# Optimization experiments

Hardware: AMD Instinct MI355X
Metric: run time of the kernel (lower is better)

The kernel has to match this reference:

```python
import jax, jax.numpy as jnp
import numpy as np
from jax import lax

C, NH, HC, HID, P = 192, 8, 64, 512, 16
B, H, W = 2, 128, 128
EPS = 1e-5


def setup_inputs() -> dict:
    key = jax.random.key(0)
    ks = jax.random.split(key, 12)
    f = lambda i, shape: jax.random.normal(ks[i], shape, jnp.float32) * 0.05
    return dict(
        x=jax.random.normal(ks[0], (B, C, H, W), jnp.float32),
        ln1_g=jnp.ones((C,), jnp.float32), ln1_b=jnp.zeros((C,), jnp.float32),
        wq=f(1, (HID, C)), wk=f(2, (HID, C)), wv=f(3, (HID, C)),
        wo=f(4, (C, HID)), bo=jnp.zeros((C,), jnp.float32),
        dw_w=f(5, (C, 1, 3, 3)), dw_b=jnp.zeros((C,), jnp.float32),
        mlp_w=f(6, (C, 2 * C)), mlp_b=jnp.zeros((C,), jnp.float32),
        ln2_g=jnp.ones((C,), jnp.float32), ln2_b=jnp.zeros((C,), jnp.float32),
        c1_w=f(7, (C, C)), c1_b=jnp.zeros((C,), jnp.float32),
        res_w=f(8, (C, 1, 3, 3)), res_b=jnp.zeros((C,), jnp.float32),
        c2_w=f(9, (C, C)), c2_b=jnp.zeros((C,), jnp.float32),
    )


def ln_ch(x, g, b):
    # LayerNorm over the channel dim of an NCHW tensor (biased variance, like torch)
    m = x.mean(1, keepdims=True)
    v = ((x - m) ** 2).mean(1, keepdims=True)
    return (x - m) / jnp.sqrt(v + EPS) * g[None, :, None, None] + b[None, :, None, None]


def inorm(x):
    # InstanceNorm2d, affine=False
    m = x.mean((2, 3), keepdims=True)
    v = ((x - m) ** 2).mean((2, 3), keepdims=True)
    return (x - m) / jnp.sqrt(v + EPS)


def conv1x1(x, w, b=None):
    y = jnp.einsum('oc,bchw->bohw', w, x)
    return y if b is None else y + b[None, :, None, None]


def dwconv(x, w, b):
    y = lax.conv_general_dilated(x, w, (1, 1), 'SAME',
                                 feature_group_count=x.shape[1],
                                 dimension_numbers=('NCHW', 'OIHW', 'NCHW'))
    return y + b[None, :, None, None]


def res_block(x, w, b):
    return jax.nn.gelu(inorm(dwconv(x, w, b)), approximate=False) + x


def dpsa(x, ln_g, ln_b, wq, wk, wv, wo, bo):
    Bs, _, Hs, Ws = x.shape
    xn = ln_ch(x, ln_g, ln_b)

    def proj(w):  # -> (B*NH, H, W, HC)
        t = jnp.einsum('oc,bchw->bohw', w, xn)
        return t.reshape(Bs * NH, HC, Hs, Ws).transpose(0, 2, 3, 1)

    l2n = lambda t: t / jnp.maximum(jnp.linalg.norm(t, axis=-1, keepdims=True), 1e-12)
    q = l2n(proj(wq))
    k = l2n(proj(wk))
    v = proj(wv)

    qs = q.sum((1, 2))                                   # (BH, HC)
    h_scores = jnp.einsum('bc,bhc->bh', qs, k.sum(2))    # (BH, H)
    w_scores = jnp.einsum('bc,bwc->bw', qs, k.sum(1))    # (BH, W)
    _, h_idx = lax.top_k(h_scores, P)
    _, w_idx = lax.top_k(w_scores, P)

    k = jnp.take_along_axis(k, h_idx[:, :, None, None], axis=1)   # (BH, P, W, HC)
    v = jnp.take_along_axis(v, h_idx[:, :, None, None], axis=1)
    k = jnp.take_along_axis(k, w_idx[:, None, :, None], axis=2)   # (BH, P, P, HC)
    v = jnp.take_along_axis(v, w_idx[:, None, :, None], axis=2)

    qf = q.reshape(Bs * NH, Hs * Ws, HC)
    kf = k.reshape(Bs * NH, P * P, HC)
    vf = v.reshape(Bs * NH, P * P, HC)
    attn = jax.nn.softmax(jnp.einsum('bqc,bkc->bqk', qf, kf), axis=-1)
    out = jnp.einsum('bqk,bkc->bqc', attn, vf)
    out = out.reshape(Bs, NH, Hs, Ws, HC).transpose(0, 1, 4, 2, 3).reshape(Bs, NH * HC, Hs, Ws)
    return conv1x1(out, wo, bo)


def reference(x, ln1_g, ln1_b, wq, wk, wv, wo, bo, dw_w, dw_b, mlp_w, mlp_b,
              ln2_g, ln2_b, c1_w, c1_b, res_w, res_b, c2_w, c2_b):
    global_branch = dpsa(x, ln1_g, ln1_b, wq, wk, wv, wo, bo)
    local_branch = dwconv(x, dw_w, dw_b)
    f = jnp.concatenate((local_branch, global_branch), axis=1)
    f = conv1x1(f, mlp_w, mlp_b) + x
    y = ln_ch(f, ln2_g, ln2_b)
    y = jax.nn.gelu(inorm(conv1x1(y, c1_w, c1_b)), approximate=False)
    y = res_block(y, res_w, res_b)
    y = inorm(conv1x1(y, c2_w, c2_b))
    return y
```

## Files before the change

### kernel.cpp

```cpp
#include <hip/hip_runtime.h>
#include <math.h>

constexpr int kC   = 192;
constexpr int kNH  = 8;
constexpr int kHC  = 64;
constexpr int kHID = 512;
constexpr int kP   = 16;
constexpr int kB   = 2;
constexpr int kH   = 128;
constexpr int kW   = 128;
constexpr int kHW  = kH * kW;
constexpr int kN   = kB * kHW;
constexpr float kEPS = 1e-5f;

typedef __attribute__((ext_vector_type(8))) short bf16x8;
typedef __attribute__((ext_vector_type(4))) float f32x4;

__device__ inline unsigned short f2bf(float f) {
    unsigned int u = __builtin_bit_cast(unsigned int, f);
    unsigned int r = (u + 0x7FFFu + ((u >> 16) & 1u)) >> 16;
    return (unsigned short)r;
}
__device__ inline float bf2f(unsigned short u) {
    return __builtin_bit_cast(float, (unsigned int)u << 16);
}
__device__ inline unsigned int cvtpk(float lo, float hi) {
    unsigned int r;
    asm("v_cvt_pk_bf16_f32 %0, %1, %2" : "=v"(r) : "v"(lo), "v"(hi));
    return r;
}
__device__ inline unsigned long long pk4(float a, float b, float c, float d) {
    return (unsigned long long)cvtpk(a, b) | ((unsigned long long)cvtpk(c, d) << 32);
}
__device__ inline f32x4 ubf4(unsigned long long u) {
    f32x4 r;
    r[0] = bf2f((unsigned short)u);
    r[1] = bf2f((unsigned short)(u >> 16));
    r[2] = bf2f((unsigned short)(u >> 32));
    r[3] = bf2f((unsigned short)(u >> 48));
    return r;
}
__device__ inline float gelu_f(float x) {
    return 0.5f * x * (1.0f + erff(x * 0.70710678118654752f));
}

__global__ void prep_kernel(float* __restrict__ zbase,
                            const float* wq, const float* wk, const float* wm,
                            const float* c1, const float* c2,
                            const float* wo, const float* mlp_b, const float* bo,
                            unsigned short* wqb, unsigned short* wkb,
                            unsigned short* mlpb1, unsigned short* c1b, unsigned short* c2b,
                            unsigned short* w2pb, float* bp2)
{
    int i = blockIdx.x * 256 + threadIdx.x;
    if (i < 2304) { zbase[i] = 0.f; return; }
    i -= 2304;
    if (i < 98304) { wqb[i] = f2bf(wq[i]); return; }
    i -= 98304;
    if (i < 98304) { wkb[i] = f2bf(wk[i]); return; }
    i -= 98304;
    if (i < 36864) { int o = i / 192, k = i - o * 192; mlpb1[i] = f2bf(wm[o * 384 + k]); return; }
    i -= 36864;
    if (i < 36864) { c1b[i] = f2bf(c1[i]); return; }
    i -= 36864;
    if (i < 36864) { c2b[i] = f2bf(c2[i]); return; }
    i -= 36864;
    if (i < 98304) {
        int o = i >> 9, j = i & 511;
        const float* a = wm + o * 384 + 192;
        float s = 0.f;
        for (int c = 0; c < 192; ++c) s += a[c] * wo[c * 512 + j];
        w2pb[o * 512 + j] = f2bf(s);
        if (j == 0) {
            float t = mlp_b[o];
            for (int c = 0; c < 192; ++c) t += a[c] * bo[c];
            bp2[o] = t;
        }
    }
}

__global__ __launch_bounds__(256) void txln_kernel(const float* __restrict__ x,
                                                   unsigned short* __restrict__ xpb,
                                                   unsigned short* __restrict__ xnb,
                                                   const float* __restrict__ g,
                                                   const float* __restrict__ bb)
{
    __shared__ float tile[192][65];
    __shared__ float red[2][4][64];
    __shared__ float pms[64], prs[64];
    int hw0 = blockIdx.x * 64;
    int b   = blockIdx.y;
    int tid = threadIdx.x;
    for (int i = tid; i < 192 * 64; i += 256) {
        int c = i >> 6, p = i & 63;
        tile[c][p] = x[(size_t)(b * kC + c) * kHW + hw0 + p];
    }
    __syncthreads();
    {
        int p = tid & 63, qt = tid >> 6;
        float s = 0.f, ss = 0.f;
        for (int c = qt * 48; c < qt * 48 + 48; ++c) {
            float v = tile[c][p]; s += v; ss += v * v;
        }
        red[0][qt][p] = s; red[1][qt][p] = ss;
    }
    __syncthreads();
    if (tid < 64) {
        float s  = red[0][0][tid] + red[0][1][tid] + red[0][2][tid] + red[0][3][tid];
        float ss = red[1][0][tid] + red[1][1][tid] + red[1][2][tid] + red[1][3][tid];
        float m = s * (1.0f / kC);
        float var = ss * (1.0f / kC) - m * m;
        pms[tid] = m;
        prs[tid] = rsqrtf(var + kEPS);
    }
    __syncthreads();
    for (int i = tid; i < 64 * 192; i += 256) {
        int p = i / 192, c = i - p * 192;
        float raw = tile[c][p];
        size_t oi = (size_t)(b * kHW + hw0 + p) * kC + c;
        xpb[oi] = f2bf(raw);
        xnb[oi] = f2bf((raw - pms[p]) * prs[p] * g[c] + bb[c]);
    }
}

#define MGEMM_CORE(KVAL, APTR, BPTR)                                              \
    {                                                                             \
        const unsigned short* Ap = APTR;                                          \
        const unsigned short* Bp = BPTR;                                          \
        _Pragma("unroll 2")                                                       \
        for (int k = 0; k < KVAL; k += 32) {                                      \
            bf16x8 a0 = *(const bf16x8*)(Ap + k);                                 \
            bf16x8 a1 = *(const bf16x8*)(Ap + (size_t)16 * KVAL + k);             \
            bf16x8 b0 = *(const bf16x8*)(Bp + k);                                 \
            bf16x8 b1 = *(const bf16x8*)(Bp + (size_t)16 * KVAL + k);             \
            bf16x8 b2 = *(const bf16x8*)(Bp + (size_t)32 * KVAL + k);             \
            bf16x8 b3 = *(const bf16x8*)(Bp + (size_t)48 * KVAL + k);             \
            acc[0][0] = __builtin_amdgcn_mfma_f32_16x16x32_bf16(a0, b0, acc[0][0], 0, 0, 0); \
            acc[0][1] = __builtin_amdgcn_mfma_f32_16x16x32_bf16(a0, b1, acc[0][1], 0, 0, 0); \
            acc[0][2] = __builtin_amdgcn_mfma_f32_16x16x32_bf16(a0, b2, acc[0][2], 0, 0, 0); \
            acc[0][3] = __builtin_amdgcn_mfma_f32_16x16x32_bf16(a0, b3, acc[0][3], 0, 0, 0); \
            acc[1][0] = __builtin_amdgcn_mfma_f32_16x16x32_bf16(a1, b0, acc[1][0], 0, 0, 0); \
            acc[1][1] = __builtin_amdgcn_mfma_f32_16x16x32_bf16(a1, b1, acc[1][1], 0, 0, 0); \
            acc[1][2] = __builtin_amdgcn_mfma_f32_16x16x32_bf16(a1, b2, acc[1][2], 0, 0, 0); \
            acc[1][3] = __builtin_amdgcn_mfma_f32_16x16x32_bf16(a1, b3, acc[1][3], 0, 0, 0); \
        }                                                                         \
    }

__global__ __launch_bounds__(256) void qk_proj_kernel(
    const unsigned short* __restrict__ wqb, const unsigned short* __restrict__ wkb,
    const unsigned short* __restrict__ xnb,
    unsigned short* __restrict__ qpb, unsigned short* __restrict__ kpb,
    float* __restrict__ qpart, float* __restrict__ ksum_h)
{
    __shared__ float rbuf[2][2][4][4][4];
    int bid = blockIdx.x;
    int xcd = bid & 7;
    int idx = bid >> 3;
    int nblk = xcd * 32 + (idx & 31);
    int hpz  = idx >> 5;
    int hp = hpz & 3, isK = hpz >> 2;

    int nB = nblk * 128;
    const unsigned short* A = isK ? wkb : wqb;
    unsigned short* out = isK ? kpb : qpb;
    float* red_out = isK ? ksum_h : qpart;

    int w = threadIdx.x >> 6, lane = threadIdx.x & 63;
    int l15 = lane & 15, g = lane >> 4;
    int wm = w & 1, wn = w >> 1;
    int oB = hp * 128;

    const unsigned short* Ap = A + (size_t)(oB + wm * 64 + l15) * 192 + 8 * g;
    const unsigned short* Bp = xnb + (size_t)(nB + wn * 64 + l15) * 192 + 8 * g;

    f32x4 acc[4][4];
#pragma unroll
    for (int mt = 0; mt < 4; ++mt)
#pragma unroll
        for (int nt = 0; nt < 4; ++nt) acc[mt][nt] = (f32x4){0.f,0.f,0.f,0.f};

#pragma unroll 2
    for (int k = 0; k < 192; k += 32) {
        bf16x8 a[4], bb[4];
#pragma unroll
        for (int mt = 0; mt < 4; ++mt) a[mt] = *(const bf16x8*)(Ap + (size_t)mt * 16 * 192 + k);
#pragma unroll
        for (int nt = 0; nt < 4; ++nt) bb[nt] = *(const bf16x8*)(Bp + (size_t)nt * 16 * 192 + k);
#pragma unroll
        for (int mt = 0; mt < 4; ++mt)
#pragma unroll
            for (int nt = 0; nt < 4; ++nt)
                acc[mt][nt] = __builtin_amdgcn_mfma_f32_16x16x32_bf16(a[mt], bb[nt], acc[mt][nt], 0, 0, 0);
    }

    float sc[4];
#pragma unroll
    for (int nt = 0; nt < 4; ++nt) {
        float s = 0.f;
#pragma unroll
        for (int mt = 0; mt < 4; ++mt) {
            f32x4 a = acc[mt][nt];
            s += (a[0]*a[0] + a[1]*a[1]) + (a[2]*a[2] + a[3]*a[3]);
        }
        s += __shfl_xor(s, 16);
        s += __shfl_xor(s, 32);
        sc[nt] = 1.0f / fmaxf(sqrtf(s), 1e-12f);
    }

#pragma unroll
    for (int nt = 0; nt < 4; ++nt) {
        int n = nB + wn * 64 + nt * 16 + l15;
#pragma unroll
        for (int mt = 0; mt < 4; ++mt) {
            int o = oB + wm * 64 + mt * 16 + 4 * g;
            f32x4 v = acc[mt][nt];
            *(unsigned long long*)(out + (size_t)n * kHID + o) =
                pk4(v[0]*sc[nt], v[1]*sc[nt], v[2]*sc[nt], v[3]*sc[nt]);
        }
    }

    float sred[4][4] = {};
#pragma unroll
    for (int nt = 0; nt < 4; ++nt)
#pragma unroll
        for (int mt = 0; mt < 4; ++mt) {
            f32x4 a = acc[mt][nt];
            sred[mt][0] += a[0] * sc[nt];
            sred[mt][1] += a[1] * sc[nt];
            sred[mt][2] += a[2] * sc[nt];
            sred[mt][3] += a[3] * sc[nt];
        }
#pragma unroll
    for (int off = 1; off < 16; off <<= 1)
#pragma unroll
        for (int mt = 0; mt < 4; ++mt)
#pragma unroll
            for (int r = 0; r < 4; ++r)
                sred[mt][r] += __shfl_xor(sred[mt][r], off);
    if (l15 == 0)
#pragma unroll
        for (int mt = 0; mt < 4; ++mt)
#pragma unroll
            for (int r = 0; r < 4; ++r)
                rbuf[wm][wn][g][mt][r] = sred[mt][r];
    __syncthreads();
    if (threadIdx.x < 128) {
        int wm2 = threadIdx.x >> 6;
        int o = threadIdx.x & 63;
        int mt2 = o >> 4, g2 = (o >> 2) & 3, r2 = o & 3;
        float v = rbuf[wm2][0][g2][mt2][r2] + rbuf[wm2][1][g2][mt2][r2];
        int row = (nB & (kHW - 1)) >> 7;
        int b = nB >> 14;
        int bh = b * 8 + hp * 2 + wm2;
        red_out[((size_t)(bh * 128 + row)) * 64 + o] = v;
    }
}

__global__ void dwconv_pm_kernel(const unsigned short* __restrict__ in,
                                 unsigned short* __restrict__ out,
                                 const float* __restrict__ wt, const float* __restrict__ bias)
{
    int idx = blockIdx.x * 256 + threadIdx.x;
    int n = idx / 48;
    int c0 = (idx - n * 48) * 4;
    int hw = n & (kHW - 1);
    int h = hw >> 7, ww = hw & 127;
    f32x4 s = *(const f32x4*)(bias + c0);
#pragma unroll
    for (int dy = -1; dy <= 1; ++dy) {
        int hh = h + dy;
        if (hh < 0 || hh >= kH) continue;
#pragma unroll
        for (int dx = -1; dx <= 1; ++dx) {
            int wx = ww + dx;
            if (wx < 0 || wx >= kW) continue;
            f32x4 v = ubf4(*(const unsigned long long*)(in + (size_t)(n + dy * kW + dx) * kC + c0));
            int t = (dy + 1) * 3 + (dx + 1);
            s[0] += v[0] * wt[(c0 + 0) * 9 + t];
            s[1] += v[1] * wt[(c0 + 1) * 9 + t];
            s[2] += v[2] * wt[(c0 + 2) * 9 + t];
            s[3] += v[3] * wt[(c0 + 3) * 9 + t];
        }
    }
    *(unsigned long long*)(out + (size_t)n * kC + c0) = pk4(s[0], s[1], s[2], s[3]);
}

__global__ void sum_h_kernel(const unsigned short* __restrict__ buf, float* __restrict__ out)
{
    __shared__ float red[4][64];
    int w = blockIdx.x, bh = blockIdx.y;
    int hc = threadIdx.x & 63, seg = threadIdx.x >> 6;
    int b = bh >> 3, nh = bh & 7;
    const unsigned short* p = buf + (size_t)(b * kHW + seg * 32 * kW + w) * kHID + nh * kHC + hc;
    float s = 0.f;
    for (int h = 0; h < 32; ++h) s += bf2f(p[(size_t)h * kW * kHID]);
    red[seg][hc] = s;
    __syncthreads();
    if (threadIdx.x < 64)
        out[((size_t)bh * kW + w) * kHC + threadIdx.x] =
            red[0][threadIdx.x] + red[1][threadIdx.x] + red[2][threadIdx.x] + red[3][threadIdx.x];
}

__global__ __launch_bounds__(256) void mgemm_is_kernel(
    const unsigned short* __restrict__ A, const unsigned short* __restrict__ B,
    unsigned short* __restrict__ out, const float* __restrict__ bias,
    float* __restrict__ accp)
{
    __shared__ float sa[2][64], qa[2][64];
    int bid = blockIdx.x;
    int xcd = bid & 7;
    int idx = bid >> 3;
    int nB = (xcd * 32 + (idx & 31)) * 128;
    int oB = (idx >> 5) * 64;
    int w = threadIdx.x >> 6, lane = threadIdx.x & 63;
    int l15 = lane & 15, g = lane >> 4;
    int wm = w & 1, wn = w >> 1;

    f32x4 acc[2][4];
#pragma unroll
    for (int mt = 0; mt < 2; ++mt)
#pragma unroll
        for (int nt = 0; nt < 4; ++nt) acc[mt][nt] = (f32x4){0.f,0.f,0.f,0.f};

    MGEMM_CORE(192, A + (size_t)(oB + wm * 32 + l15) * 192 + 8 * g,
                    B + (size_t)(nB + wn * 64 + l15) * 192 + 8 * g);

    f32x4 vv[2][4];
#pragma unroll
    for (int mt = 0; mt < 2; ++mt)
#pragma unroll
        for (int nt = 0; nt < 4; ++nt) {
            int o = oB + wm * 32 + mt * 16 + 4 * g;
            int n = nB + wn * 64 + nt * 16 + l15;
            f32x4 v = acc[mt][nt] + *(const f32x4*)(bias + o);
            vv[mt][nt] = v;
            *(unsigned long long*)(out + (size_t)n * kC + o) = pk4(v[0], v[1], v[2], v[3]);
        }
    float s2[2][4] = {}, q2[2][4] = {};
#pragma unroll
    for (int mt = 0; mt < 2; ++mt)
#pragma unroll
        for (int nt = 0; nt < 4; ++nt)
#pragma unroll
            for (int r = 0; r < 4; ++r) {
                float v = vv[mt][nt][r];
                s2[mt][r] += v; q2[mt][r] += v * v;
            }
#pragma unroll
    for (int off = 1; off < 16; off <<= 1)
#pragma unroll
        for (int mt = 0; mt < 2; ++mt)
#pragma unroll
            for (int r = 0; r < 4; ++r) {
                s2[mt][r] += __shfl_xor(s2[mt][r], off);
                q2[mt][r] += __shfl_xor(q2[mt][r], off);
            }
    if (l15 == 0)
#pragma unroll
        for (int mt = 0; mt < 2; ++mt)
#pragma unroll
            for (int r = 0; r < 4; ++r) {
                int ol = wm * 32 + mt * 16 + 4 * g + r;
                sa[wn][ol] = s2[mt][r];
                qa[wn][ol] = q2[mt][r];
            }
    __syncthreads();
    if (threadIdx.x < 128) {
        int ol = threadIdx.x & 63, st = threadIdx.x >> 6;
        float v = st ? (qa[0][ol] + qa[1][ol]) : (sa[0][ol] + sa[1][ol]);
        int b = nB >> 14;
        atomicAdd(&accp[(size_t)(b * kC + oB + ol) * 2 + st], v);
    }
}

__global__ __launch_bounds__(384) void mgemm_mlp_ln_kernel(
    const unsigned short* __restrict__ A1, const unsigned short* __restrict__ B1,
    const unsigned short* __restrict__ A2, const unsigned short* __restrict__ B2,
    unsigned short* __restrict__ out, const float* __restrict__ bp2,
    const unsigned short* __restrict__ res,
    const float* __restrict__ lng, const float* __restrict__ lnb)
{
    __shared__ float lnS[3][2][4][16], lnQ[3][2][4][16];
    int bid = blockIdx.x;
    int nB = ((bid & 7) * 32 + (bid >> 3)) * 128;
    int w = threadIdx.x >> 6, lane = threadIdx.x & 63;
    int l15 = lane & 15, g = lane >> 4;
    int om = w >> 1, on = w & 1;
    int oB = om * 64;

    f32x4 acc[4][4];
#pragma unroll
    for (int mt = 0; mt < 4; ++mt)
#pragma unroll
        for (int nt = 0; nt < 4; ++nt) acc[mt][nt] = (f32x4){0.f,0.f,0.f,0.f};

    {
        const unsigned short* Ap = A1 + (size_t)(oB + l15) * 192 + 8 * g;
        const unsigned short* Bp = B1 + (size_t)(nB + on * 64 + l15) * 192 + 8 * g;
#pragma unroll 2
        for (int k = 0; k < 192; k += 32) {
            bf16x8 a[4], bb[4];
#pragma unroll
            for (int mt = 0; mt < 4; ++mt) a[mt] = *(const bf16x8*)(Ap + (size_t)mt * 16 * 192 + k);
#pragma unroll
            for (int nt = 0; nt < 4; ++nt) bb[nt] = *(const bf16x8*)(Bp + (size_t)nt * 16 * 192 + k);
#pragma unroll
            for (int mt = 0; mt < 4; ++mt)
#pragma unroll
                for (int nt = 0; nt < 4; ++nt)
                    acc[mt][nt] = __builtin_amdgcn_mfma_f32_16x16x32_bf16(a[mt], bb[nt], acc[mt][nt], 0, 0, 0);
        }
    }
    {
        const unsigned short* Ap = A2 + (size_t)(oB + l15) * 512 + 8 * g;
        const unsigned short* Bp = B2 + (size_t)(nB + on * 64 + l15) * 512 + 8 * g;
#pragma unroll 2
        for (int k = 0; k < 512; k += 32) {
            bf16x8 a[4], bb[4];
#pragma unroll
            for (int mt = 0; mt < 4; ++mt) a[mt] = *(const bf16x8*)(Ap + (size_t)mt * 16 * 512 + k);
#pragma unroll
            for (int nt = 0; nt < 4; ++nt) bb[nt] = *(const bf16x8*)(Bp + (size_t)nt * 16 * 512 + k);
#pragma unroll
            for (int mt = 0; mt < 4; ++mt)
#pragma unroll
                for (int nt = 0; nt < 4; ++nt)
                    acc[mt][nt] = __builtin_amdgcn_mfma_f32_16x16x32_bf16(a[mt], bb[nt], acc[mt][nt], 0, 0, 0);
        }
    }

    float sp[4] = {}, sq[4] = {};
#pragma unroll
    for (int nt = 0; nt < 4; ++nt) {
        int n = nB + on * 64 + nt * 16 + l15;
#pragma unroll
        for (int mt = 0; mt < 4; ++mt) {
            int o = oB + mt * 16 + 4 * g;
            f32x4 v = acc[mt][nt];
            v[0] += bp2[o]; v[1] += bp2[o+1]; v[2] += bp2[o+2]; v[3] += bp2[o+3];
            v += ubf4(*(const unsigned long long*)(res + (size_t)n * kC + o));
            acc[mt][nt] = v;
            sp[nt] += (v[0] + v[1]) + (v[2] + v[3]);
            sq[nt] += (v[0]*v[0] + v[1]*v[1]) + (v[2]*v[2] + v[3]*v[3]);
        }
    }
#pragma unroll
    for (int nt = 0; nt < 4; ++nt) {
        sp[nt] += __shfl_xor(sp[nt], 16);
        sp[nt] += __shfl_xor(sp[nt], 32);
        sq[nt] += __shfl_xor(sq[nt], 16);
        sq[nt] += __shfl_xor(sq[nt], 32);
    }
    if (g == 0)
#pragma unroll
        for (int nt = 0; nt < 4; ++nt) {
            lnS[om][on][nt][l15] = sp[nt];
            lnQ[om][on][nt][l15] = sq[nt];
        }
    __syncthreads();

#pragma unroll
    for (int nt = 0; nt < 4; ++nt) {
        float S = lnS[0][on][nt][l15] + lnS[1][on][nt][l15] + lnS[2][on][nt][l15];
        float Q = lnQ[0][on][nt][l15] + lnQ[1][on][nt][l15] + lnQ[2][on][nt][l15];
        float m = S * (1.0f / kC);
        float var = Q * (1.0f / kC) - m * m;
        float rs = rsqrtf(var + kEPS);
        int n = nB + on * 64 + nt * 16 + l15;
#pragma unroll
        for (int mt = 0; mt < 4; ++mt) {
            int o = oB + mt * 16 + 4 * g;
            f32x4 v = acc[mt][nt];
            f32x4 gg = *(const f32x4*)(lng + o);
            f32x4 bv = *(const f32x4*)(lnb + o);
            *(unsigned long long*)(out + (size_t)n * kC + o) =
                pk4((v[0]-m)*rs*gg[0] + bv[0], (v[1]-m)*rs*gg[1] + bv[1],
                    (v[2]-m)*rs*gg[2] + bv[2], (v[3]-m)*rs*gg[3] + bv[3]);
        }
    }
}

__global__ void score_topk_kernel(const float* __restrict__ qpart,
                                  const float* __restrict__ ksum_h,
                                  const float* __restrict__ ksum_w,
                                  int* __restrict__ hidx, int* __restrict__ widx)
{
    __shared__ float qsl[2][64];
    __shared__ float hs[128], ws[128];
    int bh = blockIdx.x;
    int tid = threadIdx.x;
    int hc = tid & 63, grp = tid >> 6;
    {
        const float* qp = qpart + ((size_t)bh * 128 + grp * 64) * 64 + hc;
        float s = 0.f;
        for (int i = 0; i < 64; ++i) s += qp[(size_t)i * 64];
        qsl[grp][hc] = s;
    }
    __syncthreads();
    if (tid < 64) qsl[0][tid] += qsl[1][tid];
    __syncthreads();
    {
        const float* kh = ksum_h + ((size_t)bh * 128 + tid) * 64;
        const float* kw = ksum_w + ((size_t)bh * 128 + tid) * 64;
        float sh = 0.f, sw = 0.f;
        for (int c = 0; c < 64; ++c) {
            float q = qsl[0][c];
            sh += q * kh[c];
            sw += q * kw[c];
        }
        hs[tid] = sh; ws[tid] = sw;
    }
    __syncthreads();
    int sel = tid >> 6;
    const float* sc = sel ? ws : hs;
    int* out = (sel ? widx : hidx) + bh * kP;
    int lane = tid & 63;
    float v0 = sc[lane], v1 = sc[lane + 64];
    int i0 = lane, i1 = lane + 64;
    for (int p = 0; p < kP; ++p) {
        float bv; int bi;
        if (v1 > v0) { bv = v1; bi = i1; } else { bv = v0; bi = i0; }
#pragma unroll
        for (int off = 1; off < 64; off <<= 1) {
            float ov = __shfl_xor(bv, off);
            int   oi = __shfl_xor(bi, off);
            if (ov > bv || (ov == bv && oi < bi)) { bv = ov; bi = oi; }
        }
        if (lane == 0) out[p] = bi;
        if (i0 == bi) v0 = -INFINITY;
        if (i1 == bi) v1 = -INFINITY;
    }
}

__global__ void gather_kv_kernel(const unsigned short* __restrict__ kpb,
                                 const unsigned short* __restrict__ xnb,
                                 const float* __restrict__ wv,
                                 const int* __restrict__ hidx, const int* __restrict__ widx,
                                 unsigned short* __restrict__ kf, unsigned short* __restrict__ vfT)
{
    int bh = blockIdx.y, p1 = blockIdx.x;
    int b = bh >> 3, nh = bh & 7;
    int hc = threadIdx.x & 63, pg = threadIdx.x >> 6;
    int hrow = hidx[bh * kP + p1];
    int o = nh * kHC + hc;
    const float* wvp = wv + (size_t)o * kC;
    for (int p2 = pg; p2 < kP; p2 += 4) {
        int wcol = widx[bh * kP + p2];
        int n = b * kHW + hrow * kW + wcol;
        int kidx = p1 * kP + p2;
        kf[((size_t)bh * 256 + kidx) * 64 + hc] = kpb[(size_t)n * kHID + nh * kHC + hc];
        const unsigned int* xr = (const unsigned int*)(xnb + (size_t)n * kC);
        float s = 0.f;
        for (int c2 = 0; c2 < kC / 2; ++c2) {
            unsigned int u = xr[c2];
            s += wvp[c2 * 2]     * bf2f((unsigned short)(u & 0xffff));
            s += wvp[c2 * 2 + 1] * bf2f((unsigned short)(u >> 16));
        }
        vfT[((size_t)bh * 64 + hc) * 256 + kidx] = f2bf(s);
    }
}

__global__ __launch_bounds__(256) void attn_kernel(
    const unsigned short* __restrict__ qpb, unsigned short* __restrict__ ob,
    const unsigned short* __restrict__ kf, const unsigned short* __restrict__ vfT)
{
    __shared__ unsigned short pls[64 * 256];
    __shared__ float lred[4][4][16];

    int bid = blockIdx.x;
    int xcd = bid & 7;
    int idx = bid >> 3;
    int bh = xcd * 2 + (idx >> 7);
    int qblk = idx & 127;
    int b = bh >> 3, nh = bh & 7;
    int nbase = b * kHW + qblk * 128;
    int tid = threadIdx.x;
    int w = tid >> 6, lane = tid & 63, l15 = lane & 15, g = lane >> 4;

    const unsigned short* kfb = kf + (size_t)bh * 256 * 64;
    bf16x8 ak[4][2];
#pragma unroll
    for (int mt = 0; mt < 4; ++mt)
#pragma unroll
        for (int kt = 0; kt < 2; ++kt)
            ak[mt][kt] = *(const bf16x8*)&kfb[(size_t)(w * 64 + mt * 16 + l15) * 64 + kt * 32 + 8 * g];

    const unsigned short* vfb = vfT + (size_t)bh * 64 * 256;

#pragma unroll
    for (int sub = 0; sub < 2; ++sub) {
        int n0 = nbase + sub * 64;
        bf16x8 bq[4][2];
#pragma unroll
        for (int nt = 0; nt < 4; ++nt)
#pragma unroll
            for (int kt = 0; kt < 2; ++kt)
                bq[nt][kt] = *(const bf16x8*)(qpb + (size_t)(n0 + nt * 16 + l15) * kHID
                                              + nh * kHC + kt * 32 + 8 * g);

        f32x4 acc[4][4];
#pragma unroll
        for (int mt = 0; mt < 4; ++mt)
#pragma unroll
            for (int nt = 0; nt < 4; ++nt) acc[mt][nt] = (f32x4){0.f,0.f,0.f,0.f};

#pragma unroll
        for (int kt = 0; kt < 2; ++kt)
#pragma unroll
            for (int mt = 0; mt < 4; ++mt)
#pragma unroll
                for (int nt = 0; nt < 4; ++nt)
                    acc[mt][nt] = __builtin_amdgcn_mfma_f32_16x16x32_bf16(
                        ak[mt][kt], bq[nt][kt], acc[mt][nt], 0, 0, 0);

        if (sub) __syncthreads();

        float lpart[4] = {0.f, 0.f, 0.f, 0.f};
#pragma unroll
        for (int mt = 0; mt < 4; ++mt)
#pragma unroll
            for (int nt = 0; nt < 4; ++nt) {
                float e0 = __expf(acc[mt][nt][0]);
                float e1 = __expf(acc[mt][nt][1]);
                float e2 = __expf(acc[mt][nt][2]);
                float e3 = __expf(acc[mt][nt][3]);
                lpart[nt] += (e0 + e1) + (e2 + e3);
                int qq = nt * 16 + l15;
                int k0 = w * 64 + mt * 16 + 4 * g;
                int kx = k0 ^ ((qq & 7) << 3);
                *(unsigned long long*)&pls[qq * 256 + kx] = pk4(e0, e1, e2, e3);
            }
#pragma unroll
        for (int nt = 0; nt < 4; ++nt) {
            lpart[nt] += __shfl_xor(lpart[nt], 16);
            lpart[nt] += __shfl_xor(lpart[nt], 32);
        }
        if (g == 0)
#pragma unroll
            for (int nt = 0; nt < 4; ++nt) lred[w][nt][l15] = lpart[nt];
        __syncthreads();

        f32x4 oacc[4];
#pragma unroll
        for (int nt = 0; nt < 4; ++nt) oacc[nt] = (f32x4){0.f,0.f,0.f,0.f};

#pragma unroll
        for (int ks = 0; ks < 8; ++ks) {
            bf16x8 av = *(const bf16x8*)&vfb[(size_t)(w * 16 + l15) * 256 + ks * 32 + 8 * g];
#pragma unroll
            for (int nt = 0; nt < 4; ++nt) {
                int qq = nt * 16 + l15;
                int kx = (ks * 32 + 8 * g) ^ ((qq & 7) << 3);
                bf16x8 bp = *(const bf16x8*)&pls[qq * 256 + kx];
                oacc[nt] = __builtin_amdgcn_mfma_f32_16x16x32_bf16(av, bp, oacc[nt], 0, 0, 0);
            }
        }

#pragma unroll
        for (int nt = 0; nt < 4; ++nt) {
            float l = lred[0][nt][l15] + lred[1][nt][l15] + lred[2][nt][l15] + lred[3][nt][l15];
            float inv = 1.0f / l;
            int qq = nt * 16 + l15;
            int hc0 = w * 16 + 4 * g;
            *(unsigned long long*)(ob + (size_t)(n0 + qq) * kHID + nh * kHC + hc0) =
                pk4(oacc[nt][0] * inv, oacc[nt][1] * inv, oacc[nt][2] * inv, oacc[nt][3] * inv);
        }
    }
}

__global__ void istats_bf16_kernel(const unsigned short* __restrict__ in, float* __restrict__ acc)
{
    int n0 = blockIdx.x * 64;
    int b = n0 >> 14;
    int c = threadIdx.x;
    float s = 0.f, ss = 0.f;
    for (int p = 0; p < 64; ++p) {
        float v = bf2f(in[(size_t)(n0 + p) * kC + c]);
        s += v; ss += v * v;
    }
    atomicAdd(&acc[(size_t)(b * kC + c) * 2],     s);
    atomicAdd(&acc[(size_t)(b * kC + c) * 2 + 1], ss);
}

__device__ inline void inorm_ms(const float* acc, int b, int c, float& m, float& rs)
{
    float s  = acc[(size_t)(b * kC + c) * 2];
    float ss = acc[(size_t)(b * kC + c) * 2 + 1];
    m = s * (1.0f / kHW);
    float var = ss * (1.0f / kHW) - m * m;
    rs = rsqrtf(var + kEPS);
}

template<int MODE>
__global__ void apply_pm_kernel(const unsigned short* __restrict__ in, const float* __restrict__ acc,
                                unsigned short* __restrict__ out, const unsigned short* __restrict__ addsrc)
{
    int idx = blockIdx.x * 256 + threadIdx.x;
    int n = idx / 48;
    int c0 = (idx - n * 48) * 4;
    int b = n >> 14;
    f32x4 v = ubf4(*(const unsigned long long*)(in + (size_t)n * kC + c0));
    f32x4 r;
#pragma unroll
    for (int j = 0; j < 4; ++j) {
        float m, rs;
        inorm_ms(acc, b, c0 + j, m, rs);
        float x = (v[j] - m) * rs;
        r[j] = gelu_f(x);
    }
    if (MODE == 1)
        r += ubf4(*(const unsigned long long*)(addsrc + (size_t)n * kC + c0));
    *(unsigned long long*)(out + (size_t)n * kC + c0) = pk4(r[0], r[1], r[2], r[3]);
}

__global__ __launch_bounds__(256) void final_kernel(const unsigned short* __restrict__ in,
                                                    const float* __restrict__ acc,
                                                    float* __restrict__ out)
{
    __shared__ unsigned short tile[192][68];
    int n0 = blockIdx.x * 64;
    int b = n0 >> 14;
    int hw0 = n0 & (kHW - 1);
    int tid = threadIdx.x;
    for (int i = tid; i < 64 * 48; i += 256) {
        int p = i / 48, cq = i - p * 48;
        unsigned long long u = *(const unsigned long long*)(in + (size_t)(n0 + p) * kC + cq * 4);
        tile[cq * 4 + 0][p] = (unsigned short)u;
        tile[cq * 4 + 1][p] = (unsigned short)(u >> 16);
        tile[cq * 4 + 2][p] = (unsigned short)(u >> 32);
        tile[cq * 4 + 3][p] = (unsigned short)(u >> 48);
    }
    __syncthreads();
    for (int i = tid; i < 192 * 16; i += 256) {
        int c = i >> 4, grp = i & 15;
        float m, rs;
        inorm_ms(acc, b, c, m, rs);
        f32x4 o;
#pragma unroll
        for (int j = 0; j < 4; ++j)
            o[j] = (bf2f(tile[c][grp * 4 + j]) - m) * rs;
        *(f32x4*)(out + (size_t)(b * kC + c) * kHW + hw0 + grp * 4) = o;
    }
}

extern "C" void kernel_launch(void* const* d_in, const int* in_sizes, int n_in,
                              void* d_out, int out_size, void* d_ws, size_t ws_size,
                              hipStream_t stream)
{
    const float* x     = (const float*)d_in[0];
    const float* ln1_g = (const float*)d_in[1];
    const float* ln1_b = (const float*)d_in[2];
    const float* wq    = (const float*)d_in[3];
    const float* wk    = (const float*)d_in[4];
    const float* wv    = (const float*)d_in[5];
    const float* wo    = (const float*)d_in[6];
    const float* bo    = (const float*)d_in[7];
    const float* dw_w  = (const float*)d_in[8];
    const float* dw_b  = (const float*)d_in[9];
    const float* mlp_w = (const float*)d_in[10];
    const float* mlp_b = (const float*)d_in[11];
    const float* ln2_g = (const float*)d_in[12];
    const float* ln2_b = (const float*)d_in[13];
    const float* c1_w  = (const float*)d_in[14];
    const float* c1_b  = (const float*)d_in[15];
    const float* res_w = (const float*)d_in[16];
    const float* res_b = (const float*)d_in[17];
    const float* c2_w  = (const float*)d_in[18];
    const float* c2_b  = (const float*)d_in[19];

    char* base = (char*)d_ws;
    unsigned short* XPb = (unsigned short*)(base);
    unsigned short* XNb = (unsigned short*)(base + 25165824);
    unsigned short* QPb = (unsigned short*)(base + 37748736);
    unsigned short* T2  = QPb;
    unsigned short* KPb = (unsigned short*)(base + 71303168);
    unsigned short* OB  = KPb;
    unsigned short* Y2  = KPb;
    unsigned short* LB  = (unsigned short*)(base + 104857600);
    unsigned short* Y3  = LB;
    unsigned short* T1  = (unsigned short*)(base + 117440512);
    unsigned short* R   = T1;
    char* sm = base + 130023424;
    float* qpart  = (float*)(sm);                 sm += 524288;
    float* ksum_h = (float*)(sm);                 sm += 524288;
    float* ksum_w = (float*)(sm);                 sm += 524288;
    float* acc0   = (float*)(sm);                 sm += 3072;
    float* acc1   = (float*)(sm);                 sm += 3072;
    float* acc2   = (float*)(sm);                 sm += 3072;
    unsigned short* kf   = (unsigned short*)(sm); sm += 524288;
    unsigned short* vfT  = (unsigned short*)(sm); sm += 524288;
    unsigned short* wqb  = (unsigned short*)(sm); sm += 196608;
    unsigned short* wkb  = (unsigned short*)(sm); sm += 196608;
    unsigned short* mlpb1= (unsigned short*)(sm); sm += 73728;
    unsigned short* c1b  = (unsigned short*)(sm); sm += 73728;
    unsigned short* c2b  = (unsigned short*)(sm); sm += 73728;
    unsigned short* w2pb = (unsigned short*)(sm); sm += 196608;
    float* bp2 = (float*)(sm);                    sm += 1024;
    int* hidx = (int*)(sm);                       sm += 1024;
    int* widx = (int*)(sm);

    prep_kernel<<<1593, 256, 0, stream>>>(acc0, wq, wk, mlp_w, c1_w, c2_w,
                                          wo, mlp_b, bo,
                                          wqb, wkb, mlpb1, c1b, c2b, w2pb, bp2);
    txln_kernel<<<dim3(kHW / 64, kB), 256, 0, stream>>>(x, XPb, XNb, ln1_g, ln1_b);
    qk_proj_kernel<<<2048, 256, 0, stream>>>(wqb, wkb, XNb, QPb, KPb, qpart, ksum_h);
    dwconv_pm_kernel<<<(kN * 48) / 256, 256, 0, stream>>>(XPb, LB, dw_w, dw_b);
    sum_h_kernel<<<dim3(kW, 16), 256, 0, stream>>>(KPb, ksum_w);
    score_topk_kernel<<<16, 128, 0, stream>>>(qpart, ksum_h, ksum_w, hidx, widx);
    gather_kv_kernel<<<dim3(kP, 16), 256, 0, stream>>>(KPb, XNb, wv, hidx, widx, kf, vfT);
    attn_kernel<<<2048, 256, 0, stream>>>(QPb, OB, kf, vfT);
    mgemm_mlp_ln_kernel<<<kN / 128, 384, 0, stream>>>(mlpb1, LB, w2pb, OB, XNb, bp2, XPb,
                                                      ln2_g, ln2_b);
    mgemm_is_kernel<<<768, 256, 0, stream>>>(c1b, XNb, T1, c1_b, acc0);
    apply_pm_kernel<0><<<(kN * 48) / 256, 256, 0, stream>>>(T1, acc0, Y2, nullptr);
    dwconv_pm_kernel<<<(kN * 48) / 256, 256, 0, stream>>>(Y2, R, res_w, res_b);
    istats_bf16_kernel<<<kN / 64, 192, 0, stream>>>(R, acc1);
    apply_pm_kernel<1><<<(kN * 48) / 256, 256, 0, stream>>>(R, acc1, Y3, Y2);
    mgemm_is_kernel<<<768, 256, 0, stream>>>(c2b, Y3, T2, c2_b, acc2);
    final_kernel<<<kN / 64, 256, 0, stream>>>(T2, acc2, (float*)d_out);
}
```

Measured before the change: 447.5 us.

## Stop materializing K projection; compute column sums in-GEMM and recompute gathered K

The qk projection kernel no longer writes the full normalized K tensor. It adds a third block kind that recomputes K over column-strided pixel tiles so the per-column sums come straight out of the GEMM reduction, and the separate sum_h kernel is removed. The gather kernel now recomputes the selected K rows from wk and the normalized input, with an in-wave L2 normalization. This drops a large bf16 write and two strided reads in exchange for redoing the K GEMM once more, with strided B loads in that pass.

New measurement: 470.9 us. +5.2%, slower.

```diff
diff --git a/kernel.cpp b/kernel.cpp
--- a/kernel.cpp
+++ b/kernel.cpp
@@ -149,29 +149,39 @@
 __global__ __launch_bounds__(256) void qk_proj_kernel(
     const unsigned short* __restrict__ wqb, const unsigned short* __restrict__ wkb,
     const unsigned short* __restrict__ xnb,
-    unsigned short* __restrict__ qpb, unsigned short* __restrict__ kpb,
-    float* __restrict__ qpart, float* __restrict__ ksum_h)
+    unsigned short* __restrict__ qpb,
+    float* __restrict__ qpart, float* __restrict__ ksum_h, float* __restrict__ ksum_w)
 {
     __shared__ float rbuf[2][2][4][4][4];
     int bid = blockIdx.x;
     int xcd = bid & 7;
     int idx = bid >> 3;
-    int nblk = xcd * 32 + (idx & 31);
-    int hpz  = idx >> 5;
-    int hp = hpz & 3, isK = hpz >> 2;
-
-    int nB = nblk * 128;
-    const unsigned short* A = isK ? wkb : wqb;
-    unsigned short* out = isK ? kpb : qpb;
-    float* red_out = isK ? ksum_h : qpart;
-
-    int w = threadIdx.x >> 6, lane = threadIdx.x & 63;
+    int kind = idx >> 7;
+    int sub = idx & 127;
+    int hp = sub >> 5;
+
+    int wid = threadIdx.x >> 6, lane = threadIdx.x & 63;
     int l15 = lane & 15, g = lane >> 4;
-    int wm = w & 1, wn = w >> 1;
+    int wm = wid & 1, wn = wid >> 1;
     int oB = hp * 128;
 
+    const unsigned short* A = (kind == 0) ? wqb : wkb;
     const unsigned short* Ap = A + (size_t)(oB + wm * 64 + l15) * 192 + 8 * g;
-    const unsigned short* Bp = xnb + (size_t)(nB + wn * 64 + l15) * 192 + 8 * g;
+
+    int nBq = 0, wcol = 0, bimg = 0;
+    size_t pix0, rstep;
+    if (kind < 2) {
+        nBq = (xcd * 32 + (sub & 31)) * 128;
+        pix0 = (size_t)(nBq + wn * 64 + l15);
+        rstep = 1;
+    } else {
+        wcol = xcd * 16 + (sub & 15);
+        bimg = (sub >> 4) & 1;
+        pix0 = (size_t)bimg * kHW + (size_t)(wn * 64 + l15) * kW + wcol;
+        rstep = kW;
+    }
+    const unsigned short* Bp = xnb + pix0 * kC + 8 * g;
+    const size_t r16 = (size_t)16 * rstep * kC;
 
     f32x4 acc[4][4];
 #pragma unroll
@@ -181,16 +191,16 @@
 
 #pragma unroll 2
     for (int k = 0; k < 192; k += 32) {
-        bf16x8 a[4], bb[4];
+        bf16x8 a[4], bv[4];
 #pragma unroll
         for (int mt = 0; mt < 4; ++mt) a[mt] = *(const bf16x8*)(Ap + (size_t)mt * 16 * 192 + k);
 #pragma unroll
-        for (int nt = 0; nt < 4; ++nt) bb[nt] = *(const bf16x8*)(Bp + (size_t)nt * 16 * 192 + k);
+        for (int nt = 0; nt < 4; ++nt) bv[nt] = *(const bf16x8*)(Bp + (size_t)nt * r16 + k);
 #pragma unroll
         for (int mt = 0; mt < 4; ++mt)
 #pragma unroll
             for (int nt = 0; nt < 4; ++nt)
-                acc[mt][nt] = __builtin_amdgcn_mfma_f32_16x16x32_bf16(a[mt], bb[nt], acc[mt][nt], 0, 0, 0);
+                acc[mt][nt] = __builtin_amdgcn_mfma_f32_16x16x32_bf16(a[mt], bv[nt], acc[mt][nt], 0, 0, 0);
     }
 
     float sc[4];
@@ -207,15 +217,17 @@
         sc[nt] = 1.0f / fmaxf(sqrtf(s), 1e-12f);
     }
 
-#pragma unroll
-    for (int nt = 0; nt < 4; ++nt) {
-        int n = nB + wn * 64 + nt * 16 + l15;
-#pragma unroll
-        for (int mt = 0; mt < 4; ++mt) {
-            int o = oB + wm * 64 + mt * 16 + 4 * g;
-            f32x4 v = acc[mt][nt];
-            *(unsigned long long*)(out + (size_t)n * kHID + o) =
-                pk4(v[0]*sc[nt], v[1]*sc[nt], v[2]*sc[nt], v[3]*sc[nt]);
+    if (kind == 0) {
+#pragma unroll
+        for (int nt = 0; nt < 4; ++nt) {
+            int n = nBq + wn * 64 + nt * 16 + l15;
+#pragma unroll
+            for (int mt = 0; mt < 4; ++mt) {
+                int o = oB + wm * 64 + mt * 16 + 4 * g;
+                f32x4 v = acc[mt][nt];
+                *(unsigned long long*)(qpb + (size_t)n * kHID + o) =
+                    pk4(v[0]*sc[nt], v[1]*sc[nt], v[2]*sc[nt], v[3]*sc[nt]);
+            }
         }
     }
 
@@ -245,14 +257,20 @@
                 rbuf[wm][wn][g][mt][r] = sred[mt][r];
     __syncthreads();
     if (threadIdx.x < 128) {
+        float* red_out = (kind == 0) ? qpart : (kind == 1 ? ksum_h : ksum_w);
         int wm2 = threadIdx.x >> 6;
         int o = threadIdx.x & 63;
         int mt2 = o >> 4, g2 = (o >> 2) & 3, r2 = o & 3;
         float v = rbuf[wm2][0][g2][mt2][r2] + rbuf[wm2][1][g2][mt2][r2];
-        int row = (nB & (kHW - 1)) >> 7;
-        int b = nB >> 14;
-        int bh = b * 8 + hp * 2 + wm2;
-        red_out[((size_t)(bh * 128 + row)) * 64 + o] = v;
+        int bh, rowIdx;
+        if (kind < 2) {
+            rowIdx = (nBq & (kHW - 1)) >> 7;
+            bh = (nBq >> 14) * 8 + hp * 2 + wm2;
+        } else {
+            rowIdx = wcol;
+            bh = bimg * 8 + hp * 2 + wm2;
+        }
+        red_out[((size_t)(bh * 128 + rowIdx)) * 64 + o] = v;
     }
 }
 
@@ -283,22 +301,6 @@
         }
     }
     *(unsigned long long*)(out + (size_t)n * kC + c0) = pk4(s[0], s[1], s[2], s[3]);
-}
-
-__global__ void sum_h_kernel(const unsigned short* __restrict__ buf, float* __restrict__ out)
-{
-    __shared__ float red[4][64];
-    int w = blockIdx.x, bh = blockIdx.y;
-    int hc = threadIdx.x & 63, seg = threadIdx.x >> 6;
-    int b = bh >> 3, nh = bh & 7;
-    const unsigned short* p = buf + (size_t)(b * kHW + seg * 32 * kW + w) * kHID + nh * kHC + hc;
-    float s = 0.f;
-    for (int h = 0; h < 32; ++h) s += bf2f(p[(size_t)h * kW * kHID]);
-    red[seg][hc] = s;
-    __syncthreads();
-    if (threadIdx.x < 64)
-        out[((size_t)bh * kW + w) * kHC + threadIdx.x] =
-            red[0][threadIdx.x] + red[1][threadIdx.x] + red[2][threadIdx.x] + red[3][threadIdx.x];
 }
 
 __global__ __launch_bounds__(256) void mgemm_is_kernel(
@@ -532,7 +534,7 @@
     }
 }
 
-__global__ void gather_kv_kernel(const unsigned short* __restrict__ kpb,
+__global__ void gather_kv_kernel(const unsigned short* __restrict__ wkb,
                                  const unsigned short* __restrict__ xnb,
                                  const float* __restrict__ wv,
                                  const int* __restrict__ hidx, const int* __restrict__ widx,
@@ -544,19 +546,29 @@
     int hrow = hidx[bh * kP + p1];
     int o = nh * kHC + hc;
     const float* wvp = wv + (size_t)o * kC;
+    const unsigned short* wkp = wkb + (size_t)o * kC;
     for (int p2 = pg; p2 < kP; p2 += 4) {
         int wcol = widx[bh * kP + p2];
         int n = b * kHW + hrow * kW + wcol;
         int kidx = p1 * kP + p2;
-        kf[((size_t)bh * 256 + kidx) * 64 + hc] = kpb[(size_t)n * kHID + nh * kHC + hc];
         const unsigned int* xr = (const unsigned int*)(xnb + (size_t)n * kC);
-        float s = 0.f;
+        const unsigned int* kr = (const unsigned int*)wkp;
+        float sv = 0.f, sk = 0.f;
         for (int c2 = 0; c2 < kC / 2; ++c2) {
             unsigned int u = xr[c2];
-            s += wvp[c2 * 2]     * bf2f((unsigned short)(u & 0xffff));
-            s += wvp[c2 * 2 + 1] * bf2f((unsigned short)(u >> 16));
-        }
-        vfT[((size_t)bh * 64 + hc) * 256 + kidx] = f2bf(s);
+            float x0 = bf2f((unsigned short)(u & 0xffff));
+            float x1 = bf2f((unsigned short)(u >> 16));
+            sv += wvp[c2 * 2] * x0 + wvp[c2 * 2 + 1] * x1;
+            unsigned int kw2 = kr[c2];
+            sk += bf2f((unsigned short)(kw2 & 0xffff)) * x0
+                + bf2f((unsigned short)(kw2 >> 16)) * x1;
+        }
+        float ss = sk * sk;
+#pragma unroll
+        for (int off = 1; off < 64; off <<= 1) ss += __shfl_xor(ss, off);
+        float sc = 1.0f / fmaxf(sqrtf(ss), 1e-12f);
+        kf[((size_t)bh * 256 + kidx) * 64 + hc] = f2bf(sk * sc);
+        vfT[((size_t)bh * 64 + hc) * 256 + kidx] = f2bf(sv);
     }
 }
 
@@ -773,9 +785,8 @@
     unsigned short* XNb = (unsigned short*)(base + 25165824);
     unsigned short* QPb = (unsigned short*)(base + 37748736);
     unsigned short* T2  = QPb;
-    unsigned short* KPb = (unsigned short*)(base + 71303168);
-    unsigned short* OB  = KPb;
-    unsigned short* Y2  = KPb;
+    unsigned short* OB  = (unsigned short*)(base + 71303168);
+    unsigned short* Y2  = OB;
     unsigned short* LB  = (unsigned short*)(base + 104857600);
     unsigned short* Y3  = LB;
     unsigned short* T1  = (unsigned short*)(base + 117440512);
@@ -803,11 +814,10 @@
                                           wo, mlp_b, bo,
                                           wqb, wkb, mlpb1, c1b, c2b, w2pb, bp2);
     txln_kernel<<<dim3(kHW / 64, kB), 256, 0, stream>>>(x, XPb, XNb, ln1_g, ln1_b);
-    qk_proj_kernel<<<2048, 256, 0, stream>>>(wqb, wkb, XNb, QPb, KPb, qpart, ksum_h);
+    qk_proj_kernel<<<3072, 256, 0, stream>>>(wqb, wkb, XNb, QPb, qpart, ksum_h, ksum_w);
     dwconv_pm_kernel<<<(kN * 48) / 256, 256, 0, stream>>>(XPb, LB, dw_w, dw_b);
-    sum_h_kernel<<<dim3(kW, 16), 256, 0, stream>>>(KPb, ksum_w);
     score_topk_kernel<<<16, 128, 0, stream>>>(qpart, ksum_h, ksum_w, hidx, widx);
-    gather_kv_kernel<<<dim3(kP, 16), 256, 0, stream>>>(KPb, XNb, wv, hidx, widx, kf, vfT);
+    gather_kv_kernel<<<dim3(kP, 16), 256, 0, stream>>>(wkb, XNb, wv, hidx, widx, kf, vfT);
     attn_kernel<<<2048, 256, 0, stream>>>(QPb, OB, kf, vfT);
     mgemm_mlp_ln_kernel<<<kN / 128, 384, 0, stream>>>(mlpb1, LB, w2pb, OB, XNb, bp2, XPb,
                                                       ln2_g, ln2_b);
```
